# Kernel optimization log

Hardware: AMD Instinct MI355X
Metric: run time of the kernel (lower is better)

The kernel has to match this reference:

```python
import jax, jax.numpy as jnp
import numpy as np

B, S, D, H, HD = 4, 1024, 512, 8, 64  # batch, seq_len, hidden_dim, n_heads, head_dim
N_DIL = min(5, H)


def _head_masks(seq_len: int, n_heads: int) -> jnp.ndarray:
    """Log-sparse banded+dilated masks, shape [n_heads, S, S] (bool)."""
    i = jnp.arange(seq_len)
    diff = jnp.abs(i[:, None] - i[None, :])  # [S, S]
    masks = jnp.stack([
        (diff <= 2 ** h) | (diff % (2 ** (h + 1)) == 0)
        for h in range(N_DIL)
    ])  # [N_DIL, S, S]
    idx = [min(h, N_DIL - 1) for h in range(n_heads)]
    return masks[jnp.asarray(idx)]  # [H, S, S]


def setup_inputs() -> dict:
    key = jax.random.key(0)
    ks = jax.random.split(key, 9)
    sc = 0.02
    return {
        "x": jax.random.normal(ks[0], (B, S, D), jnp.float32),
        "Wq": jax.random.normal(ks[1], (H, D, HD), jnp.float32) * sc,
        "bq": jax.random.normal(ks[2], (H, HD), jnp.float32) * sc,
        "Wk": jax.random.normal(ks[3], (H, D, HD), jnp.float32) * sc,
        "bk": jax.random.normal(ks[4], (H, HD), jnp.float32) * sc,
        "Wv": jax.random.normal(ks[5], (H, D, HD), jnp.float32) * sc,
        "bv": jax.random.normal(ks[6], (H, HD), jnp.float32) * sc,
        "Wo": jax.random.normal(ks[7], (D, D), jnp.float32) * sc,
        "bo": jax.random.normal(ks[8], (D,), jnp.float32) * sc,
    }


def reference(x, Wq, bq, Wk, bk, Wv, bv, Wo, bo):
    b, s, d = x.shape
    h, _, hd = Wq.shape
    # Per-head projections (batched over heads).
    q = jnp.einsum("bsd,hde->bhse", x, Wq) + bq[None, :, None, :]
    k = jnp.einsum("bsd,hde->bhse", x, Wk) + bk[None, :, None, :]
    v = jnp.einsum("bsd,hde->bhse", x, Wv) + bv[None, :, None, :]
    scores = jnp.einsum("bhse,bhte->bhst", q, k) / (hd ** 0.5)
    mask = _head_masks(s, h)  # [H, S, S] bool; diagonal always allowed
    scores = jnp.where(mask[None], scores, -jnp.inf)
    probs = jax.nn.softmax(scores, axis=-1)  # dropout is identity in eval
    out = jnp.einsum("bhst,bhte->bhse", probs, v)
    concat = out.transpose(0, 2, 1, 3).reshape(b, s, d)  # heads concatenated
    return concat @ Wo + bo
```

## Files before the change

### kernel.cpp

```cpp
#include <hip/hip_runtime.h>

typedef unsigned short u16;
typedef unsigned int u32;
typedef __attribute__((ext_vector_type(8))) __bf16 bf16x8;
typedef __attribute__((ext_vector_type(4))) float f32x4;
typedef __attribute__((ext_vector_type(16))) float f32x16;
typedef __attribute__((ext_vector_type(4))) u32 u32x4;

#if __has_builtin(__builtin_amdgcn_exp2f)
#define EXP2F(x) __builtin_amdgcn_exp2f(x)
#else
#define EXP2F(x) exp2f(x)
#endif

#define SC_Q 0.18033688011112042f

static __device__ __forceinline__ u16 f2bf(float f) {
  unsigned u = __builtin_bit_cast(unsigned, f);
  u += 0x7fffu + ((u >> 16) & 1u);
  return (u16)(u >> 16);
}
static __device__ __forceinline__ float bf2f(u16 v) {
  return __builtin_bit_cast(float, (u32)v << 16);
}

static __device__ __forceinline__ f32x4 mfma16(bf16x8 a, bf16x8 b, f32x4 c) {
  return __builtin_amdgcn_mfma_f32_16x16x32_bf16(a, b, c, 0, 0, 0);
}
static __device__ __forceinline__ f32x16 mfma32(bf16x8 a, bf16x8 b, f32x16 c) {
  return __builtin_amdgcn_mfma_f32_32x32x16_bf16(a, b, c, 0, 0, 0);
}

static __device__ __forceinline__ u32 cvtpk(float lo, float hi_) {
  u32 r;
  asm("v_cvt_pk_bf16_f32 %0, %1, %2" : "=v"(r) : "v"(lo), "v"(hi_));
  return r;
}

static __device__ __forceinline__ void barrier_raw() {
  asm volatile("" ::: "memory");
  __builtin_amdgcn_s_barrier();
  asm volatile("" ::: "memory");
}

static __device__ __forceinline__ void gload_lds16(const u16* g, u16* l) {
  __builtin_amdgcn_global_load_lds((const __attribute__((address_space(1))) u32*)g,
                                   (__attribute__((address_space(3))) u32*)l, 16, 0, 0);
}

__global__ void pack_x_kernel(const float* __restrict__ x, u16* __restrict__ xb, int n) {
  int idx = blockIdx.x * 256 + threadIdx.x;
  if (idx < n) xb[idx] = f2bf(x[idx]);
}

__global__ void pack_w_kernel(const float* __restrict__ Wq, const float* __restrict__ Wk,
                              const float* __restrict__ Wv, const float* __restrict__ Wo,
                              const float* __restrict__ bq, const float* __restrict__ bk,
                              const float* __restrict__ bv, u16* __restrict__ BTqkv,
                              u16* __restrict__ BTo, float* __restrict__ bqkv) {
  int idx = blockIdx.x * 256 + threadIdx.x;
  if (idx < 1536 * 512) {
    int n = idx >> 9, d = idx & 511;
    int t = n >> 9, rem = n & 511;
    int h = rem >> 6, e = rem & 63;
    const float* W = (t == 0) ? Wq : ((t == 1) ? Wk : Wv);
    float sc = (t == 0) ? SC_Q : 1.0f;
    BTqkv[idx] = f2bf(W[((size_t)h * 512 + d) * 64 + e] * sc);
  } else if (idx < 1536 * 512 + 512 * 512) {
    int j = idx - 1536 * 512;
    int n = j >> 9, d = j & 511;
    BTo[j] = f2bf(Wo[(size_t)d * 512 + n]);
  } else if (idx < 1536 * 512 + 512 * 512 + 1536) {
    int j = idx - (1536 * 512 + 512 * 512);
    int t = j >> 9, rem = j & 511;
    float v = (t == 0 ? bq : (t == 1 ? bk : bv))[rem];
    bqkv[j] = v * (t == 0 ? SC_Q : 1.0f);
  }
}

__global__ __launch_bounds__(256) void gemm_qkv_kernel(const u16* __restrict__ A,
                                                       const u16* __restrict__ BT,
                                                       const float* __restrict__ bias,
                                                       u16* __restrict__ QK,
                                                       u16* __restrict__ Vt) {
  __shared__ __align__(16) u16 Al[128 * 64];
  __shared__ __align__(16) u16 Bl[64 * 64];
  const int K = 512;
  const int tid = threadIdx.x;
  const int w = tid >> 6, lane = tid & 63, g = lane >> 4, i = lane & 15;
  const int m0 = blockIdx.y * 128, n0 = blockIdx.x * 64;
  const int wr = (w >> 1) * 64, wc = (w & 1) * 32;

  f32x4 acc[4][2];
#pragma unroll
  for (int a = 0; a < 4; ++a)
#pragma unroll
    for (int b = 0; b < 2; ++b) acc[a][b] = f32x4{0.f, 0.f, 0.f, 0.f};

  const u16* agp[4];
  const u16* bgp[2];
#pragma unroll
  for (int it = 0; it < 4; ++it) {
    const int slot = it * 256 + tid;
    agp[it] = A + (size_t)(m0 + (slot >> 3)) * K + (slot & 7) * 8;
  }
#pragma unroll
  for (int it = 0; it < 2; ++it) {
    const int slot = it * 256 + tid;
    bgp[it] = BT + (size_t)(n0 + (slot >> 3)) * K + (slot & 7) * 8;
  }

  for (int k0 = 0; k0 < K; k0 += 64) {
    __syncthreads();
#pragma unroll
    for (int it = 0; it < 4; ++it) gload_lds16(agp[it] + k0, &Al[(it * 256 + tid) * 8]);
#pragma unroll
    for (int it = 0; it < 2; ++it) gload_lds16(bgp[it] + k0, &Bl[(it * 256 + tid) * 8]);
    __syncthreads();
#pragma unroll
    for (int ks = 0; ks < 2; ++ks) {
      bf16x8 af[4], bf[2];
#pragma unroll
      for (int mf = 0; mf < 4; ++mf)
        af[mf] =
            *reinterpret_cast<const bf16x8*>(&Al[(wr + mf * 16 + i) * 64 + ks * 32 + 8 * g]);
#pragma unroll
      for (int nf = 0; nf < 2; ++nf)
        bf[nf] =
            *reinterpret_cast<const bf16x8*>(&Bl[(wc + nf * 16 + i) * 64 + ks * 32 + 8 * g]);
#pragma unroll
      for (int mf = 0; mf < 4; ++mf)
#pragma unroll
        for (int nf = 0; nf < 2; ++nf) acc[mf][nf] = mfma16(af[mf], bf[nf], acc[mf][nf]);
    }
  }

  if (n0 < 1024) {
#pragma unroll
    for (int nf = 0; nf < 2; ++nf) {
      const int col = n0 + wc + nf * 16 + i;
      const float bb = bias[col];
#pragma unroll
      for (int mf = 0; mf < 4; ++mf) {
#pragma unroll
        for (int r = 0; r < 4; ++r) {
          const int row = m0 + wr + mf * 16 + 4 * g + r;
          QK[(size_t)row * 1024 + col] = f2bf(acc[mf][nf][r] + bb);
        }
      }
    }
  } else {
    const int b = m0 >> 10;
    const int s0b = (m0 & 1023) + wr;
#pragma unroll
    for (int nf = 0; nf < 2; ++nf) {
      const int col = n0 + wc + nf * 16 + i;
      const float bb = bias[col];
      const int vcol = col - 1024;
#pragma unroll
      for (int mf = 0; mf < 4; ++mf) {
        u16 pk[4];
#pragma unroll
        for (int r = 0; r < 4; ++r) pk[r] = f2bf(acc[mf][nf][r] + bb);
        const int ss = s0b + mf * 16 + 4 * g;
        *reinterpret_cast<uint2*>(&Vt[(size_t)(b * 512 + vcol) * 1024 + ss]) =
            *reinterpret_cast<const uint2*>(pk);
      }
    }
  }
}

__global__ __launch_bounds__(256) void gemm_out_kernel(const u16* __restrict__ A,
                                                       const u16* __restrict__ BT,
                                                       const float* __restrict__ bias,
                                                       float* __restrict__ Cf) {
  __shared__ __align__(16) u16 Al[128 * 64];
  __shared__ __align__(16) u16 Bl[64 * 64];
  const int K = 512;
  const int tid = threadIdx.x;
  const int w = tid >> 6, lane = tid & 63, g = lane >> 4, i = lane & 15;
  const int m0 = blockIdx.y * 128, n0 = blockIdx.x * 64;
  const int wr = (w >> 1) * 64, wc = (w & 1) * 32;

  f32x4 acc[4][2];
#pragma unroll
  for (int a = 0; a < 4; ++a)
#pragma unroll
    for (int b = 0; b < 2; ++b) acc[a][b] = f32x4{0.f, 0.f, 0.f, 0.f};

  const u16* agp[4];
  const u16* bgp[2];
#pragma unroll
  for (int it = 0; it < 4; ++it) {
    const int slot = it * 256 + tid;
    agp[it] = A + (size_t)(m0 + (slot >> 3)) * K + (slot & 7) * 8;
  }
#pragma unroll
  for (int it = 0; it < 2; ++it) {
    const int slot = it * 256 + tid;
    bgp[it] = BT + (size_t)(n0 + (slot >> 3)) * K + (slot & 7) * 8;
  }

  for (int k0 = 0; k0 < K; k0 += 64) {
    __syncthreads();
#pragma unroll
    for (int it = 0; it < 4; ++it) gload_lds16(agp[it] + k0, &Al[(it * 256 + tid) * 8]);
#pragma unroll
    for (int it = 0; it < 2; ++it) gload_lds16(bgp[it] + k0, &Bl[(it * 256 + tid) * 8]);
    __syncthreads();
#pragma unroll
    for (int ks = 0; ks < 2; ++ks) {
      bf16x8 af[4], bf[2];
#pragma unroll
      for (int mf = 0; mf < 4; ++mf)
        af[mf] =
            *reinterpret_cast<const bf16x8*>(&Al[(wr + mf * 16 + i) * 64 + ks * 32 + 8 * g]);
#pragma unroll
      for (int nf = 0; nf < 2; ++nf)
        bf[nf] =
            *reinterpret_cast<const bf16x8*>(&Bl[(wc + nf * 16 + i) * 64 + ks * 32 + 8 * g]);
#pragma unroll
      for (int mf = 0; mf < 4; ++mf)
#pragma unroll
        for (int nf = 0; nf < 2; ++nf) acc[mf][nf] = mfma16(af[mf], bf[nf], acc[mf][nf]);
    }
  }

#pragma unroll
  for (int nf = 0; nf < 2; ++nf) {
    const int col = n0 + wc + nf * 16 + i;
    const float bb = bias[col];
#pragma unroll
    for (int mf = 0; mf < 4; ++mf) {
#pragma unroll
      for (int r = 0; r < 4; ++r) {
        const int row = m0 + wr + mf * 16 + 4 * g + r;
        Cf[(size_t)row * 512 + col] = acc[mf][nf][r] + bb;
      }
    }
  }
}

__global__ __launch_bounds__(256) void attn3_kernel(const u16* __restrict__ QK,
                                                    const u16* __restrict__ Vt,
                                                    u16* __restrict__ Opart16,
                                                    float* __restrict__ mlpart) {
  __shared__ __align__(16) u16 Kl[2][4096];
  __shared__ __align__(16) u16 Vl[2][4096];

  const int tid = threadIdx.x;
  const int w = tid >> 6, lane = tid & 63;
  const int col = lane & 31, hi = lane >> 5;
  const int h = blockIdx.x;
  const int zz = blockIdx.z;
  const int b = zz >> 2, s = zz & 3;
  const int bh = b * 8 + h;
  const int q0w = blockIdx.y * 128 + w * 32;
  const int kvlo = s * 256;
  const int hm = (h < 4) ? h : 4;
  const int band = 1 << hm;
  const int modm = (2 << hm) - 1;
  const int qrow = q0w + col;

  bf16x8 qf[4];
  const size_t qoff = (size_t)(b * 1024 + qrow) * 1024 + h * 64 + 8 * hi;
#pragma unroll
  for (int et = 0; et < 4; ++et)
    qf[et] = *reinterpret_cast<const bf16x8*>(QK + qoff + 16 * et);

  float bias[16];
#pragma unroll
  for (int r = 0; r < 16; ++r) {
    int c = (r & 3) + 8 * (r >> 2) + 4 * hi;
    bias[r] = (((qrow - c) & modm) == 0) ? 0.f : -1e30f;
  }

  f32x16 accO0 = {}, accO1 = {};
  float m_run = -1e30f, l_run = 0.f;

  const int slot0 = tid, slot1 = tid + 256;
  const int kj0 = slot0 >> 3, keb0 = (slot0 & 7) ^ (kj0 & 7);
  const int kj1 = slot1 >> 3, keb1 = (slot1 & 7) ^ (kj1 & 7);
  const u16* kg0 = QK + (size_t)(b * 1024 + kj0) * 1024 + 512 + h * 64 + keb0 * 8;
  const u16* kg1 = QK + (size_t)(b * 1024 + kj1) * 1024 + 512 + h * 64 + keb1 * 8;
  const u16* vg0 = Vt + (size_t)(bh * 64 + kj0) * 1024 + keb0 * 8;
  const u16* vg1 = Vt + (size_t)(bh * 64 + kj1) * 1024 + keb1 * 8;

#define STAGE(bi, kv0)                                                  \
  do {                                                                  \
    gload_lds16(kg0 + (size_t)(kv0) * 1024, &Kl[bi][slot0 * 8]);        \
    gload_lds16(kg1 + (size_t)(kv0) * 1024, &Kl[bi][slot1 * 8]);        \
    gload_lds16(vg0 + (kv0), &Vl[bi][slot0 * 8]);                       \
    gload_lds16(vg1 + (kv0), &Vl[bi][slot1 * 8]);                       \
  } while (0)

  STAGE(0, kvlo);
  int buf = 0;

  for (int t = 0; t < 4; ++t) {
    const int kv0 = kvlo + t * 64;
    if (t < 3) {
      STAGE(buf ^ 1, kv0 + 64);
      asm volatile("s_waitcnt vmcnt(4)" ::: "memory");
    } else {
      asm volatile("s_waitcnt vmcnt(0)" ::: "memory");
    }
    barrier_raw();

    const u16* Kb = Kl[buf];
    const u16* Vb = Vl[buf];

    f32x16 s0 = {}, s1 = {};
    __builtin_amdgcn_s_setprio(1);
#pragma unroll
    for (int et = 0; et < 4; ++et) {
      const int sw = ((2 * et + hi) ^ (col & 7)) << 3;
      bf16x8 kf0 = *reinterpret_cast<const bf16x8*>(&Kb[col * 64 + sw]);
      bf16x8 kf1 = *reinterpret_cast<const bf16x8*>(&Kb[(col + 32) * 64 + sw]);
      s0 = mfma32(kf0, qf[et], s0);
      s1 = mfma32(kf1, qf[et], s1);
    }
    __builtin_amdgcn_s_setprio(0);

    float p[32];
    const int dq = qrow - kv0;
    const bool near = (q0w <= kv0 + 63 + band) && (kv0 <= q0w + 31 + band);
    if (near) {
#pragma unroll
      for (int r = 0; r < 16; ++r) {
        const int c = (r & 3) + 8 * (r >> 2) + 4 * hi;
        int d0 = dq - c, d1 = d0 - 32;
        d0 = d0 < 0 ? -d0 : d0;
        d1 = d1 < 0 ? -d1 : d1;
        p[r] = (d0 <= band) ? s0[r] : s0[r] + bias[r];
        p[r + 16] = (d1 <= band) ? s1[r] : s1[r] + bias[r];
      }
    } else {
#pragma unroll
      for (int r = 0; r < 16; ++r) {
        p[r] = s0[r] + bias[r];
        p[r + 16] = s1[r] + bias[r];
      }
    }

    float tr[16];
#pragma unroll
    for (int j = 0; j < 16; ++j) tr[j] = fmaxf(p[j], p[j + 16]);
#pragma unroll
    for (int st = 8; st >= 1; st >>= 1)
#pragma unroll
      for (int j = 0; j < st; ++j) tr[j] = fmaxf(tr[j], tr[j + st]);
    float mu = fmaxf(tr[0], __shfl_xor(tr[0], 32));

    if (__any(mu > m_run + 8.f)) {
      float mn = fmaxf(m_run, mu);
      float corr = EXP2F(m_run - mn);
      m_run = mn;
      l_run *= corr;
#pragma unroll
      for (int j = 0; j < 16; ++j) {
        accO0[j] *= corr;
        accO1[j] *= corr;
      }
    }

#pragma unroll
    for (int j = 0; j < 32; ++j) p[j] = EXP2F(p[j] - m_run);
    float ts[16];
#pragma unroll
    for (int j = 0; j < 16; ++j) ts[j] = p[j] + p[j + 16];
#pragma unroll
    for (int st = 8; st >= 1; st >>= 1)
#pragma unroll
      for (int j = 0; j < st; ++j) ts[j] += ts[j + st];
    l_run += ts[0] + __shfl_xor(ts[0], 32);

#pragma unroll
    for (int kt = 0; kt < 4; ++kt) {
      const float* pp = (kt < 2) ? p : p + 16;
      const int R = (kt & 1) * 8;
      u32 A0 = cvtpk(pp[R + 0], pp[R + 1]);
      u32 A1 = cvtpk(pp[R + 2], pp[R + 3]);
      u32 B0 = cvtpk(pp[R + 4], pp[R + 5]);
      u32 B1 = cvtpk(pp[R + 6], pp[R + 7]);
      u32 xA0 = __shfl_xor(A0, 32), xA1 = __shfl_xor(A1, 32);
      u32 xB0 = __shfl_xor(B0, 32), xB1 = __shfl_xor(B1, 32);
      u32 w0 = hi ? xB0 : A0;
      u32 w1 = hi ? xB1 : A1;
      u32 w2 = hi ? B0 : xA0;
      u32 w3 = hi ? B1 : xA1;
      u32x4 pu = {w0, w1, w2, w3};
      bf16x8 paf = __builtin_bit_cast(bf16x8, pu);
      const int jb = 2 * kt + hi;
      __builtin_amdgcn_s_setprio(1);
      {
        const int erow = col;
        bf16x8 vf = *reinterpret_cast<const bf16x8*>(&Vb[erow * 64 + ((jb ^ (erow & 7)) << 3)]);
        accO0 = mfma32(paf, vf, accO0);
      }
      {
        const int erow = 32 + col;
        bf16x8 vf = *reinterpret_cast<const bf16x8*>(&Vb[erow * 64 + ((jb ^ (erow & 7)) << 3)]);
        accO1 = mfma32(paf, vf, accO1);
      }
      __builtin_amdgcn_s_setprio(0);
    }

    barrier_raw();
    buf ^= 1;
  }
#undef STAGE

  const size_t obase = (size_t)(s * 32 + bh) * 1024 + q0w;
  if (lane < 32) {
    float2 ml2 = {m_run, l_run};
    *reinterpret_cast<float2*>(&mlpart[(obase + col) * 2]) = ml2;
  }
#pragma unroll
  for (int r = 0; r < 16; ++r) {
    const int c = (r & 3) + 8 * (r >> 2) + 4 * hi;
    u16* orow = Opart16 + (obase + c) * 64;
    orow[col] = f2bf(accO0[r]);
    orow[32 + col] = f2bf(accO1[r]);
  }
}

__global__ __launch_bounds__(256) void attn_combine_kernel(const u16* __restrict__ Opart16,
                                                           const float* __restrict__ mlpart,
                                                           u16* __restrict__ Cc) {
  const int gid = blockIdx.x * 256 + threadIdx.x;
  const int rg = gid >> 4;
  const int e0 = (gid & 15) * 4;
  float m[4], l[4];
#pragma unroll
  for (int s2 = 0; s2 < 4; ++s2) {
    float2 ml2 = *reinterpret_cast<const float2*>(&mlpart[((size_t)s2 * 32768 + rg) * 2]);
    m[s2] = ml2.x;
    l[s2] = ml2.y;
  }
  const float M = fmaxf(fmaxf(m[0], m[1]), fmaxf(m[2], m[3]));
  float L = 0.f, wsc[4];
#pragma unroll
  for (int s2 = 0; s2 < 4; ++s2) {
    wsc[s2] = EXP2F(m[s2] - M);
    L += l[s2] * wsc[s2];
  }
  float o0 = 0.f, o1 = 0.f, o2 = 0.f, o3 = 0.f;
#pragma unroll
  for (int s2 = 0; s2 < 4; ++s2) {
    uint2 raw =
        *reinterpret_cast<const uint2*>(&Opart16[((size_t)s2 * 32768 + rg) * 64 + e0]);
    o0 += bf2f((u16)(raw.x & 0xffff)) * wsc[s2];
    o1 += bf2f((u16)(raw.x >> 16)) * wsc[s2];
    o2 += bf2f((u16)(raw.y & 0xffff)) * wsc[s2];
    o3 += bf2f((u16)(raw.y >> 16)) * wsc[s2];
  }
  const float inv = 1.0f / L;
  const int bh = rg >> 10, qr = rg & 1023;
  u16 ob[4] = {f2bf(o0 * inv), f2bf(o1 * inv), f2bf(o2 * inv), f2bf(o3 * inv)};
  *reinterpret_cast<uint2*>(&Cc[(size_t)((bh >> 3) * 1024 + qr) * 512 + (bh & 7) * 64 + e0]) =
      *reinterpret_cast<const uint2*>(ob);
}

extern "C" void kernel_launch(void* const* d_in, const int* in_sizes, int n_in,
                              void* d_out, int out_size, void* d_ws, size_t ws_size,
                              hipStream_t stream) {
  const float* x = (const float*)d_in[0];
  const float* Wq = (const float*)d_in[1];
  const float* bq = (const float*)d_in[2];
  const float* Wk = (const float*)d_in[3];
  const float* bk = (const float*)d_in[4];
  const float* Wv = (const float*)d_in[5];
  const float* bv = (const float*)d_in[6];
  const float* Wo = (const float*)d_in[7];
  const float* bo = (const float*)d_in[8];
  float* out = (float*)d_out;

  char* ws = (char*)d_ws;
  u16* xb = (u16*)(ws);
  u16* BTqkv = (u16*)(ws + (4u << 20));
  u16* BTo = (u16*)(ws + (6u << 20));
  float* bqkv = (float*)(ws + (7u << 20));
  u16* QK = (u16*)(ws + (8u << 20));
  u16* Cc = (u16*)(ws + (17u << 20));
  u16* Vt = (u16*)(ws + (21u << 20));
  u16* Opart16 = (u16*)(ws + (32u << 20));
  float* mlpart = (float*)(ws + (64u << 20));

  const int NX = 4096 * 512;
  pack_x_kernel<<<(NX + 255) / 256, 256, 0, stream>>>(x, xb, NX);
  const int NW = 1536 * 512 + 512 * 512 + 1536;
  pack_w_kernel<<<(NW + 255) / 256, 256, 0, stream>>>(Wq, Wk, Wv, Wo, bq, bk, bv, BTqkv,
                                                      BTo, bqkv);

  gemm_qkv_kernel<<<dim3(24, 32), 256, 0, stream>>>(xb, BTqkv, bqkv, QK, Vt);

  attn3_kernel<<<dim3(8, 8, 16), 256, 0, stream>>>(QK, Vt, Opart16, mlpart);
  attn_combine_kernel<<<2048, 256, 0, stream>>>(Opart16, mlpart, Cc);

  gemm_out_kernel<<<dim3(8, 32), 256, 0, stream>>>(Cc, BTo, bo, out);
}
```

Baseline: 70.98 us.

## Fuse x bf16 conversion into QKV GEMM and double-buffer both GEMMs

Drops the separate pack_x kernel: the QKV GEMM now reads fp32 x directly, converts it to bf16 in registers and writes it into LDS. Both GEMMs get double-buffered LDS with prefetch of the next K tile overlapped with MFMA work, using explicit waitcnt and raw barriers. The output GEMM tile shrinks to 64x64 so it launches twice as many blocks for better CU occupancy. The cost is twice the fp32 A-tile bytes read per QKV block, plus hand-tuned vmcnt counts that must exactly match the number of outstanding loads.

```diff
diff --git a/kernel.cpp b/kernel.cpp
--- a/kernel.cpp
+++ b/kernel.cpp
@@ -46,11 +46,6 @@
 static __device__ __forceinline__ void gload_lds16(const u16* g, u16* l) {
   __builtin_amdgcn_global_load_lds((const __attribute__((address_space(1))) u32*)g,
                                    (__attribute__((address_space(3))) u32*)l, 16, 0, 0);
-}
-
-__global__ void pack_x_kernel(const float* __restrict__ x, u16* __restrict__ xb, int n) {
-  int idx = blockIdx.x * 256 + threadIdx.x;
-  if (idx < n) xb[idx] = f2bf(x[idx]);
 }
 
 __global__ void pack_w_kernel(const float* __restrict__ Wq, const float* __restrict__ Wk,
@@ -78,13 +73,13 @@
   }
 }
 
-__global__ __launch_bounds__(256) void gemm_qkv_kernel(const u16* __restrict__ A,
+__global__ __launch_bounds__(256) void gemm_qkv_kernel(const float* __restrict__ X,
                                                        const u16* __restrict__ BT,
                                                        const float* __restrict__ bias,
                                                        u16* __restrict__ QK,
                                                        u16* __restrict__ Vt) {
-  __shared__ __align__(16) u16 Al[128 * 64];
-  __shared__ __align__(16) u16 Bl[64 * 64];
+  __shared__ __align__(16) u16 Al[2][128 * 64];
+  __shared__ __align__(16) u16 Bl[2][64 * 64];
   const int K = 512;
   const int tid = threadIdx.x;
   const int w = tid >> 6, lane = tid & 63, g = lane >> 4, i = lane & 15;
@@ -97,42 +92,81 @@
 #pragma unroll
     for (int b = 0; b < 2; ++b) acc[a][b] = f32x4{0.f, 0.f, 0.f, 0.f};
 
-  const u16* agp[4];
-  const u16* bgp[2];
+  const float* xg[4];
 #pragma unroll
   for (int it = 0; it < 4; ++it) {
     const int slot = it * 256 + tid;
-    agp[it] = A + (size_t)(m0 + (slot >> 3)) * K + (slot & 7) * 8;
-  }
+    xg[it] = X + (size_t)(m0 + (slot >> 3)) * K + (slot & 7) * 8;
+  }
+  const u16* bgp[2];
 #pragma unroll
   for (int it = 0; it < 2; ++it) {
     const int slot = it * 256 + tid;
     bgp[it] = BT + (size_t)(n0 + (slot >> 3)) * K + (slot & 7) * 8;
   }
 
-  for (int k0 = 0; k0 < K; k0 += 64) {
-    __syncthreads();
-#pragma unroll
-    for (int it = 0; it < 4; ++it) gload_lds16(agp[it] + k0, &Al[(it * 256 + tid) * 8]);
-#pragma unroll
-    for (int it = 0; it < 2; ++it) gload_lds16(bgp[it] + k0, &Bl[(it * 256 + tid) * 8]);
-    __syncthreads();
+  float4 a0[4], a1[4];
+#pragma unroll
+  for (int it = 0; it < 4; ++it) {
+    a0[it] = *reinterpret_cast<const float4*>(xg[it]);
+    a1[it] = *reinterpret_cast<const float4*>(xg[it] + 4);
+  }
+#pragma unroll
+  for (int it = 0; it < 2; ++it) gload_lds16(bgp[it], &Bl[0][(it * 256 + tid) * 8]);
+  asm volatile("s_waitcnt vmcnt(2)" ::: "memory");
+#pragma unroll
+  for (int it = 0; it < 4; ++it) {
+    u32x4 pk = {cvtpk(a0[it].x, a0[it].y), cvtpk(a0[it].z, a0[it].w),
+                cvtpk(a1[it].x, a1[it].y), cvtpk(a1[it].z, a1[it].w)};
+    *reinterpret_cast<u32x4*>(&Al[0][(it * 256 + tid) * 8]) = pk;
+  }
+  asm volatile("s_waitcnt lgkmcnt(0)" ::: "memory");
+
+  int cur = 0;
+  for (int t = 0; t < 8; ++t) {
+    const int k0 = t * 64;
+    if (t < 7) {
+#pragma unroll
+      for (int it = 0; it < 4; ++it) {
+        a0[it] = *reinterpret_cast<const float4*>(xg[it] + k0 + 64);
+        a1[it] = *reinterpret_cast<const float4*>(xg[it] + k0 + 68);
+      }
+#pragma unroll
+      for (int it = 0; it < 2; ++it)
+        gload_lds16(bgp[it] + k0 + 64, &Bl[cur ^ 1][(it * 256 + tid) * 8]);
+      asm volatile("s_waitcnt vmcnt(10)" ::: "memory");
+    } else {
+      asm volatile("s_waitcnt vmcnt(0)" ::: "memory");
+    }
+    barrier_raw();
 #pragma unroll
     for (int ks = 0; ks < 2; ++ks) {
       bf16x8 af[4], bf[2];
 #pragma unroll
       for (int mf = 0; mf < 4; ++mf)
-        af[mf] =
-            *reinterpret_cast<const bf16x8*>(&Al[(wr + mf * 16 + i) * 64 + ks * 32 + 8 * g]);
+        af[mf] = *reinterpret_cast<const bf16x8*>(
+            &Al[cur][(wr + mf * 16 + i) * 64 + ks * 32 + 8 * g]);
 #pragma unroll
       for (int nf = 0; nf < 2; ++nf)
-        bf[nf] =
-            *reinterpret_cast<const bf16x8*>(&Bl[(wc + nf * 16 + i) * 64 + ks * 32 + 8 * g]);
+        bf[nf] = *reinterpret_cast<const bf16x8*>(
+            &Bl[cur][(wc + nf * 16 + i) * 64 + ks * 32 + 8 * g]);
 #pragma unroll
       for (int mf = 0; mf < 4; ++mf)
 #pragma unroll
         for (int nf = 0; nf < 2; ++nf) acc[mf][nf] = mfma16(af[mf], bf[nf], acc[mf][nf]);
     }
+    if (t < 7) {
+      asm volatile("s_waitcnt vmcnt(2)" ::: "memory");
+#pragma unroll
+      for (int it = 0; it < 4; ++it) {
+        u32x4 pk = {cvtpk(a0[it].x, a0[it].y), cvtpk(a0[it].z, a0[it].w),
+                    cvtpk(a1[it].x, a1[it].y), cvtpk(a1[it].z, a1[it].w)};
+        *reinterpret_cast<u32x4*>(&Al[cur ^ 1][(it * 256 + tid) * 8]) = pk;
+      }
+      asm volatile("s_waitcnt lgkmcnt(0)" ::: "memory");
+    }
+    barrier_raw();
+    cur ^= 1;
   }
 
   if (n0 < 1024) {
@@ -174,64 +208,74 @@
                                                        const u16* __restrict__ BT,
                                                        const float* __restrict__ bias,
                                                        float* __restrict__ Cf) {
-  __shared__ __align__(16) u16 Al[128 * 64];
-  __shared__ __align__(16) u16 Bl[64 * 64];
+  __shared__ __align__(16) u16 Al[2][64 * 64];
+  __shared__ __align__(16) u16 Bl[2][64 * 64];
   const int K = 512;
   const int tid = threadIdx.x;
   const int w = tid >> 6, lane = tid & 63, g = lane >> 4, i = lane & 15;
-  const int m0 = blockIdx.y * 128, n0 = blockIdx.x * 64;
-  const int wr = (w >> 1) * 64, wc = (w & 1) * 32;
-
-  f32x4 acc[4][2];
-#pragma unroll
-  for (int a = 0; a < 4; ++a)
+  const int m0 = blockIdx.y * 64, n0 = blockIdx.x * 64;
+  const int wr = (w >> 1) * 32, wc = (w & 1) * 32;
+
+  f32x4 acc[2][2];
+#pragma unroll
+  for (int a = 0; a < 2; ++a)
 #pragma unroll
     for (int b = 0; b < 2; ++b) acc[a][b] = f32x4{0.f, 0.f, 0.f, 0.f};
 
-  const u16* agp[4];
+  const u16* agp[2];
   const u16* bgp[2];
 #pragma unroll
-  for (int it = 0; it < 4; ++it) {
+  for (int it = 0; it < 2; ++it) {
     const int slot = it * 256 + tid;
     agp[it] = A + (size_t)(m0 + (slot >> 3)) * K + (slot & 7) * 8;
-  }
-#pragma unroll
-  for (int it = 0; it < 2; ++it) {
-    const int slot = it * 256 + tid;
     bgp[it] = BT + (size_t)(n0 + (slot >> 3)) * K + (slot & 7) * 8;
   }
 
-  for (int k0 = 0; k0 < K; k0 += 64) {
-    __syncthreads();
-#pragma unroll
-    for (int it = 0; it < 4; ++it) gload_lds16(agp[it] + k0, &Al[(it * 256 + tid) * 8]);
-#pragma unroll
-    for (int it = 0; it < 2; ++it) gload_lds16(bgp[it] + k0, &Bl[(it * 256 + tid) * 8]);
-    __syncthreads();
+#define OSTAGE(bi, k0)                                              \
+  do {                                                              \
+    _Pragma("unroll") for (int it = 0; it < 2; ++it) {              \
+      gload_lds16(agp[it] + (k0), &Al[bi][(it * 256 + tid) * 8]);   \
+      gload_lds16(bgp[it] + (k0), &Bl[bi][(it * 256 + tid) * 8]);   \
+    }                                                               \
+  } while (0)
+
+  OSTAGE(0, 0);
+  int cur = 0;
+  for (int t = 0; t < 8; ++t) {
+    if (t < 7) {
+      OSTAGE(cur ^ 1, t * 64 + 64);
+      asm volatile("s_waitcnt vmcnt(4)" ::: "memory");
+    } else {
+      asm volatile("s_waitcnt vmcnt(0)" ::: "memory");
+    }
+    barrier_raw();
 #pragma unroll
     for (int ks = 0; ks < 2; ++ks) {
-      bf16x8 af[4], bf[2];
-#pragma unroll
-      for (int mf = 0; mf < 4; ++mf)
-        af[mf] =
-            *reinterpret_cast<const bf16x8*>(&Al[(wr + mf * 16 + i) * 64 + ks * 32 + 8 * g]);
+      bf16x8 af[2], bf[2];
+#pragma unroll
+      for (int mf = 0; mf < 2; ++mf)
+        af[mf] = *reinterpret_cast<const bf16x8*>(
+            &Al[cur][(wr + mf * 16 + i) * 64 + ks * 32 + 8 * g]);
 #pragma unroll
       for (int nf = 0; nf < 2; ++nf)
-        bf[nf] =
-            *reinterpret_cast<const bf16x8*>(&Bl[(wc + nf * 16 + i) * 64 + ks * 32 + 8 * g]);
-#pragma unroll
-      for (int mf = 0; mf < 4; ++mf)
+        bf[nf] = *reinterpret_cast<const bf16x8*>(
+            &Bl[cur][(wc + nf * 16 + i) * 64 + ks * 32 + 8 * g]);
+#pragma unroll
+      for (int mf = 0; mf < 2; ++mf)
 #pragma unroll
         for (int nf = 0; nf < 2; ++nf) acc[mf][nf] = mfma16(af[mf], bf[nf], acc[mf][nf]);
     }
-  }
+    barrier_raw();
+    cur ^= 1;
+  }
+#undef OSTAGE
 
 #pragma unroll
   for (int nf = 0; nf < 2; ++nf) {
     const int col = n0 + wc + nf * 16 + i;
     const float bb = bias[col];
 #pragma unroll
-    for (int mf = 0; mf < 4; ++mf) {
+    for (int mf = 0; mf < 2; ++mf) {
 #pragma unroll
       for (int r = 0; r < 4; ++r) {
         const int row = m0 + wr + mf * 16 + 4 * g + r;
@@ -477,7 +521,6 @@
   float* out = (float*)d_out;
 
   char* ws = (char*)d_ws;
-  u16* xb = (u16*)(ws);
   u16* BTqkv = (u16*)(ws + (4u << 20));
   u16* BTo = (u16*)(ws + (6u << 20));
   float* bqkv = (float*)(ws + (7u << 20));
@@ -487,16 +530,14 @@
   u16* Opart16 = (u16*)(ws + (32u << 20));
   float* mlpart = (float*)(ws + (64u << 20));
 
-  const int NX = 4096 * 512;
-  pack_x_kernel<<<(NX + 255) / 256, 256, 0, stream>>>(x, xb, NX);
   const int NW = 1536 * 512 + 512 * 512 + 1536;
   pack_w_kernel<<<(NW + 255) / 256, 256, 0, stream>>>(Wq, Wk, Wv, Wo, bq, bk, bv, BTqkv,
                                                       BTo, bqkv);
 
-  gemm_qkv_kernel<<<dim3(24, 32), 256, 0, stream>>>(xb, BTqkv, bqkv, QK, Vt);
+  gemm_qkv_kernel<<<dim3(24, 32), 256, 0, stream>>>(x, BTqkv, bqkv, QK, Vt);
 
   attn3_kernel<<<dim3(8, 8, 16), 256, 0, stream>>>(QK, Vt, Opart16, mlpart);
   attn_combine_kernel<<<2048, 256, 0, stream>>>(Opart16, mlpart, Cc);
 
-  gemm_out_kernel<<<dim3(8, 32), 256, 0, stream>>>(Cc, BTo, bo, out);
-}
+  gemm_out_kernel<<<dim3(8, 64), 256, 0, stream>>>(Cc, BTo, bo, out);
+}
```

Measured after the change: 68.58 us. 1.03x faster.
